# Kernel tuning notes

Hardware: AMD Instinct MI355X
Metric: run time of the kernel (lower is better)

Reference implementation:

```python
import jax, jax.numpy as jnp
import numpy as np

N = 50000   # nodes (single node type)
E = 200000  # edges per relation
R = 2       # relations (etypes)
D = 256     # in_dim == out_dim
H = 8       # heads
DK = D // H # 32
SQRT_DK = float(np.sqrt(DK))


def setup_inputs() -> dict:
    key = jax.random.key(0)
    ks = jax.random.split(key, 12)
    wsc = 1.0 / np.sqrt(D)   # linear-layer scale
    rsc = 1.0 / np.sqrt(DK)  # xavier-ish scale for relation tensors
    return {
        "x": jax.random.normal(ks[0], (N, D), jnp.float32),
        "src": jax.random.randint(ks[1], (R, E), 0, N, jnp.int32),
        "dst": jax.random.randint(ks[2], (R, E), 0, N, jnp.int32),
        "Wk": jax.random.normal(ks[3], (D, D), jnp.float32) * wsc,
        "bk": jnp.zeros((D,), jnp.float32),
        "Wq": jax.random.normal(ks[4], (D, D), jnp.float32) * wsc,
        "bq": jnp.zeros((D,), jnp.float32),
        "Wv": jax.random.normal(ks[5], (D, D), jnp.float32) * wsc,
        "bv": jnp.zeros((D,), jnp.float32),
        "Wa": jax.random.normal(ks[6], (D, D), jnp.float32) * wsc,
        "ba": jnp.zeros((D,), jnp.float32),
        "rel_pri": jnp.ones((R, H), jnp.float32),
        "rel_att": jax.random.normal(ks[7], (R, H, DK, DK), jnp.float32) * rsc,
        "rel_msg": jax.random.normal(ks[8], (R, H, DK, DK), jnp.float32) * rsc,
        "skip": jnp.ones((1,), jnp.float32),
    }


def reference(x, src, dst, Wk, bk, Wq, bq, Wv, bv, Wa, ba, rel_pri, rel_att, rel_msg, skip):
    # Per-type K/Q/V projections (single node type) -> [N,H,DK]
    k = (x @ Wk + bk).reshape(N, H, DK)
    q = (x @ Wq + bq).reshape(N, H, DK)
    v = (x @ Wv + bv).reshape(N, H, DK)

    # edge_attention: per-relation bmm transform of gathered src features
    key_t = jnp.einsum('rehd,rhdf->rehf', k[src], rel_att)   # [R,E,H,DK]
    val = jnp.einsum('rehd,rhdf->rehf', v[src], rel_msg)     # [R,E,H,DK]
    att = (q[dst] * key_t).sum(-1) * rel_pri[:, None, :] / SQRT_DK  # [R,E,H]

    # segment softmax over incoming edges per (relation, dst node)
    seg = (dst + N * jnp.arange(R, dtype=dst.dtype)[:, None]).reshape(-1)  # [R*E]
    att_f = att.reshape(R * E, H)
    m = jax.ops.segment_max(att_f, seg, num_segments=R * N)
    m = jnp.where(jnp.isfinite(m), m, 0.0)  # empty segments -> never gathered
    e = jnp.exp(att_f - m[seg])
    den = jax.ops.segment_sum(e, seg, num_segments=R * N)
    attn = e / den[seg]                                       # [R*E,H]

    # weighted-sum scatter aggregation, then cross_reducer='mean' over relations
    h = jax.ops.segment_sum(attn[:, :, None] * val.reshape(R * E, H, DK), seg,
                            num_segments=R * N)               # [R*N,H,DK]
    t = h.reshape(R, N, D).mean(axis=0)                        # [N,D]

    # skip-gated output projection (dropout inactive in eval, use_norm=False)
    alpha = jax.nn.sigmoid(skip[0])
    return (t @ Wa + ba) * alpha + x * (1.0 - alpha)
```

## Files before the change

kernel.cpp:

```cpp
#include <hip/hip_runtime.h>
#include <hip/hip_bf16.h>
#include <math.h>

#define NN 50000
#define EE 200000
#define DD 256
#define HH 8
#define DKK 32
#define NSEG (2 * NN)
#define SCAN_BLOCKS ((NSEG + 1023) / 1024)
#define MPAD 50048
#define LDQKV 1280
#define CAST_BLOCKS 12500
#define COUNT_BLOCKS ((2 * EE + 255) / 256)

constexpr float RSQRT_DK = 0.17677669529663687f;

__device__ __forceinline__ float bf_lo(unsigned u) { return __uint_as_float(u << 16); }
__device__ __forceinline__ float bf_hi(unsigned u) { return __uint_as_float(u & 0xffff0000u); }
__device__ __forceinline__ unsigned short f2bf(float f) {
    unsigned u = __float_as_uint(f);
    return (unsigned short)((u + 0x7fffu + ((u >> 16) & 1u)) >> 16);
}

typedef __attribute__((ext_vector_type(8))) short bf16x8;
typedef __attribute__((ext_vector_type(4))) float f32x4;
typedef __attribute__((ext_vector_type(4))) unsigned int u32x4;

#define GLDS16(g, l)                                                                   \
    __builtin_amdgcn_global_load_lds((const __attribute__((address_space(1))) unsigned int*)(g), \
                                     (__attribute__((address_space(3))) unsigned int*)(l), 16, 0, 0)

__global__ void prep_kernel(const float* __restrict__ x, unsigned short* __restrict__ xb,
                            const float* __restrict__ Wq, const float* __restrict__ Wk,
                            const float* __restrict__ Wv, const float* __restrict__ bq,
                            const float* __restrict__ bk, const float* __restrict__ bv,
                            const float* __restrict__ rel_att, const float* __restrict__ rel_msg,
                            const float* __restrict__ Wa, unsigned short* __restrict__ wa_t,
                            unsigned short* __restrict__ Wt, float* __restrict__ bb,
                            const int* __restrict__ dst, int* __restrict__ cnt) {
    if (blockIdx.x < CAST_BLOCKS) {
        const size_t i = ((size_t)blockIdx.x * 256 + threadIdx.x) * 4;
        float4 v = *(const float4*)&x[i];
        ushort4 o;
        o.x = f2bf(v.x); o.y = f2bf(v.y); o.z = f2bf(v.z); o.w = f2bf(v.w);
        *(ushort4*)&xb[i] = o;
        return;
    }
    if (blockIdx.x >= CAST_BLOCKS + 1536) {
        const int e = (blockIdx.x - CAST_BLOCKS - 1536) * 256 + threadIdx.x;
        if (e < 2 * EE) atomicAdd(&cnt[(e >= EE ? NN : 0) + dst[e]], 1);
        return;
    }
    const int n = blockIdx.x - CAST_BLOCKS, kk = threadIdx.x;
    if (n >= 1280) {
        const int nn = n - 1280;
        wa_t[(size_t)nn * 256 + kk] = f2bf(Wa[(size_t)kk * 256 + nn]);
        return;
    }
    if (n < 256) {
        Wt[(size_t)n * 256 + kk] = f2bf(Wq[(size_t)kk * 256 + n]);
        if (kk == 0) bb[n] = bq[n];
        return;
    }
    const int sec = (n - 256) >> 8;
    const int c = (n - 256) & 255;
    const int h = c >> 5, f = c & 31;
    const float* W    = (sec < 2) ? Wk : Wv;
    const float* bsrc = (sec < 2) ? bk : bv;
    const float* T = ((sec < 2) ? rel_att : rel_msg)
                   + (size_t)(sec & 1) * HH * DKK * DKK + (size_t)h * DKK * DKK + f;
    const float* wrow = &W[(size_t)kk * 256 + h * 32];
    float s = 0.f;
    #pragma unroll
    for (int d = 0; d < 32; ++d) s += wrow[d] * T[(size_t)d * 32];
    Wt[(size_t)n * 256 + kk] = f2bf(s);
    if (kk == 0) {
        float sb = 0.f;
        for (int d = 0; d < 32; ++d) sb += bsrc[h * 32 + d] * T[(size_t)d * 32];
        bb[n] = sb;
    }
}

__global__ __launch_bounds__(256) void mfma_gemm(
        const unsigned short* __restrict__ A, const unsigned short* __restrict__ Bt,
        const float* __restrict__ bias,
        unsigned short* __restrict__ Cbf, float* __restrict__ Cf,
        int M, int ldc, const float* __restrict__ xres, const float* __restrict__ skip) {
    __shared__ __align__(16) unsigned short As[3][8][64][8];
    __shared__ __align__(16) unsigned short Bs[3][8][64][8];
    const int t = threadIdx.x;
    const int w = t >> 6, l = t & 63;

    const int nwg = gridDim.x * gridDim.y;
    int lin = blockIdx.y * gridDim.x + blockIdx.x;
    {
        const int xcd = lin & 7, pos = lin >> 3;
        const int q = nwg >> 3, r = nwg & 7;
        lin = (xcd < r ? xcd * (q + 1) : r * (q + 1) + (xcd - r) * q) + pos;
    }
    const int n0 = (lin % gridDim.x) * 128;
    const int m0 = (lin / gridDim.x) * 128;
    const int wm = w & 1, wn = w >> 1;

    const int sr = l & 15, sq = l >> 4;
    const unsigned short* ga0 = A  + (size_t)(m0 + w * 16 + sr) * 256 + sq * 8;
    const unsigned short* ga1 = A  + (size_t)(m0 + (w + 4) * 16 + sr) * 256 + sq * 8;
    const unsigned short* gb0 = Bt + (size_t)(n0 + w * 16 + sr) * 256 + sq * 8;
    const unsigned short* gb1 = Bt + (size_t)(n0 + (w + 4) * 16 + sr) * 256 + sq * 8;

#define STAGE(buf, k0) do {                    \
        GLDS16(ga0 + (k0), &As[buf][w][0][0]); \
        GLDS16(ga1 + (k0), &As[buf][w + 4][0][0]); \
        GLDS16(gb0 + (k0), &Bs[buf][w][0][0]); \
        GLDS16(gb1 + (k0), &Bs[buf][w + 4][0][0]); } while (0)

    f32x4 acc[4][4];
    #pragma unroll
    for (int mi = 0; mi < 4; ++mi)
        #pragma unroll
        for (int ni = 0; ni < 4; ++ni) acc[mi][ni] = (f32x4){0.f, 0.f, 0.f, 0.f};

    STAGE(0, 0);
    STAGE(1, 32);
    #pragma unroll
    for (int it = 0; it < 8; ++it) {
        if (it < 7) { asm volatile("s_waitcnt vmcnt(4)" ::: "memory"); }
        else        { asm volatile("s_waitcnt vmcnt(0)" ::: "memory"); }
        __builtin_amdgcn_s_barrier();
        __builtin_amdgcn_sched_barrier(0);
        if (it < 6) {
            STAGE((it + 2) % 3, (it + 2) * 32);
        }
        const int b = it % 3;
        bf16x8 af[4], bfr[4];
        #pragma unroll
        for (int i = 0; i < 4; ++i) {
            af[i]  = *(const bf16x8*)&As[b][wm * 4 + i][l][0];
            bfr[i] = *(const bf16x8*)&Bs[b][wn * 4 + i][l][0];
        }
        #pragma unroll
        for (int mi = 0; mi < 4; ++mi)
            #pragma unroll
            for (int ni = 0; ni < 4; ++ni)
                acc[mi][ni] = __builtin_amdgcn_mfma_f32_16x16x32_bf16(af[mi], bfr[ni],
                                                                      acc[mi][ni], 0, 0, 0);
    }
    __syncthreads();

    unsigned short* ep = (w < 2) ? &As[0][0][0][0] : &Bs[0][0][0][0];
    ep += (w & 1) * 4096;
    const int q4 = l >> 4, c15 = l & 15;

    if (Cf == nullptr) {
        #pragma unroll
        for (int ni = 0; ni < 4; ++ni) {
            const float bcol = bias[n0 + wn * 64 + ni * 16 + c15];
            const int g = ni * 2 + (c15 >> 3);
            #pragma unroll
            for (int mi = 0; mi < 4; ++mi)
                #pragma unroll
                for (int p = 0; p < 4; ++p) {
                    const int row = mi * 16 + q4 * 4 + p;
                    ep[row * 64 + ((g ^ (row & 7)) << 3) + (c15 & 7)] =
                        f2bf(acc[mi][ni][p] + bcol);
                }
        }
        __syncthreads();
        const int rs = l >> 3, cc = l & 7;
        #pragma unroll
        for (int i = 0; i < 8; ++i) {
            const int rl = i * 8 + rs;
            const int row = m0 + wm * 64 + rl;
            if (row < M) {
                u32x4 v = *(const u32x4*)&ep[rl * 64 + ((cc ^ (rl & 7)) << 3)];
                __builtin_nontemporal_store(v,
                    (u32x4*)&Cbf[(size_t)row * (size_t)ldc + n0 + wn * 64 + cc * 8]);
            }
        }
    } else {
        const float alpha = 1.f / (1.f + __expf(-skip[0]));
        const float beta = 1.f - alpha;
        float* epf = (float*)ep;
        #pragma unroll
        for (int half = 0; half < 2; ++half) {
            __syncthreads();
            #pragma unroll
            for (int mi2 = 0; mi2 < 2; ++mi2) {
                const int mi = half * 2 + mi2;
                #pragma unroll
                for (int ni = 0; ni < 4; ++ni) {
                    const float bcol = bias[n0 + wn * 64 + ni * 16 + c15];
                    const int g = ni * 4 + (c15 >> 2);
                    #pragma unroll
                    for (int p = 0; p < 4; ++p) {
                        const int row = mi2 * 16 + q4 * 4 + p;
                        epf[row * 64 + ((g ^ (row & 7)) << 2) + (c15 & 3)] =
                            acc[mi][ni][p] + bcol;
                    }
                }
            }
            __syncthreads();
            const int cc = l & 15, rs = l >> 4;
            #pragma unroll
            for (int i = 0; i < 8; ++i) {
                const int rl = i * 4 + rs;
                const int row = m0 + wm * 64 + half * 32 + rl;
                if (row < M) {
                    const int col = n0 + wn * 64 + cc * 4;
                    float4 v = *(const float4*)&epf[rl * 64 + ((cc ^ (rl & 7)) << 2)];
                    float4 xr = *(const float4*)&xres[(size_t)row * 256 + col];
                    f32x4 o;
                    o[0] = v.x * alpha + xr.x * beta;
                    o[1] = v.y * alpha + xr.y * beta;
                    o[2] = v.z * alpha + xr.z * beta;
                    o[3] = v.w * alpha + xr.w * beta;
                    __builtin_nontemporal_store(o, (f32x4*)&Cf[(size_t)row * 256 + col]);
                }
            }
        }
    }
#undef STAGE
}

__global__ __launch_bounds__(1024) void scan_local_kernel(const int* __restrict__ cnt,
                                                          int* __restrict__ rowptr,
                                                          int* __restrict__ bsum) {
    __shared__ int sh[1024];
    const int t = threadIdx.x;
    const int idx = blockIdx.x * 1024 + t;
    const int c = (idx < NSEG) ? cnt[idx] : 0;
    sh[t] = c;
    __syncthreads();
    #pragma unroll
    for (int ofs = 1; ofs < 1024; ofs <<= 1) {
        int v = (t >= ofs) ? sh[t - ofs] : 0;
        __syncthreads();
        sh[t] += v;
        __syncthreads();
    }
    if (idx < NSEG) rowptr[idx] = sh[t] - c;
    if (t == 1023) bsum[blockIdx.x] = sh[1023];
}

__global__ __launch_bounds__(1024) void scan_add_kernel(int* __restrict__ rowptr,
                                                        const int* __restrict__ bsum,
                                                        int* __restrict__ cursor) {
    __shared__ int sb[128];
    const int t = threadIdx.x;
    if (t < 128) sb[t] = (t < SCAN_BLOCKS) ? bsum[t] : 0;
    __syncthreads();
    #pragma unroll
    for (int ofs = 1; ofs < 128; ofs <<= 1) {
        int u = 0;
        if (t < 128 && t >= ofs) u = sb[t - ofs];
        __syncthreads();
        if (t < 128) sb[t] += u;
        __syncthreads();
    }
    const int pre = sb[blockIdx.x] - bsum[blockIdx.x];
    const int idx = blockIdx.x * 1024 + t;
    if (idx < NSEG) {
        const int v = rowptr[idx] + pre;
        rowptr[idx] = v;
        cursor[idx] = v;
    }
    if (blockIdx.x == 0 && t == 127) rowptr[NSEG] = sb[127];
}

__global__ void scatter_kernel(const int* __restrict__ src, const int* __restrict__ dst,
                               int* __restrict__ cursor, int* __restrict__ csr_src) {
    int e = blockIdx.x * 256 + threadIdx.x;
    if (e >= 2 * EE) return;
    int seg = (e / EE) * NN + dst[e];
    int pos = atomicAdd(&cursor[seg], 1);
    csr_src[pos] = src[e];
}

__global__ __launch_bounds__(512) void node_agg_kernel(
        const unsigned short* __restrict__ qkv,
        const int* __restrict__ csr_src,
        const int* __restrict__ rowptr,
        const float* __restrict__ pri,
        unsigned short* __restrict__ tt_bf) {
    __shared__ float sh[4][256];
    const int w = threadIdx.x >> 6, lane = threadIdx.x & 63;
    const int nl = w >> 1, r = w & 1;
    const int n = blockIdx.x * 4 + nl;
    const int lh = lane & 31;
    const int eh = lane >> 5;
    const int h = lh >> 2;
    const size_t coff = (size_t)lh * 8;

    const uint4 qv = *(const uint4*)&qkv[(size_t)n * LDQKV + coff];
    const float q0 = bf_lo(qv.x), q1 = bf_hi(qv.x), q2 = bf_lo(qv.y), q3 = bf_hi(qv.y);
    const float q4_ = bf_lo(qv.z), q5 = bf_hi(qv.z), q6 = bf_lo(qv.w), q7 = bf_hi(qv.w);

    const float prm = pri[r * HH + h] * RSQRT_DK;
    const int seg = r * NN + n;
    const int j0 = rowptr[seg], j1 = rowptr[seg + 1];
    const size_t kbase = 256 + (size_t)r * 256 + coff;
    const size_t vbase = 768 + (size_t)r * 256 + coff;

    float a0 = 0.f, a1 = 0.f, a2 = 0.f, a3 = 0.f, a4 = 0.f, a5 = 0.f, a6 = 0.f, a7 = 0.f;
    float den = 0.f;

    int j = j0 + eh;
    uint4 kv, vv;
    bool valid = j < j1;
    if (valid) {
        const size_t rowb = (size_t)csr_src[j] * LDQKV;
        kv = *(const uint4*)&qkv[rowb + kbase];
        vv = *(const uint4*)&qkv[rowb + vbase];
    }
    while (valid) {
        const int jn = j + 2;
        const bool validn = jn < j1;
        uint4 kvn, vvn;
        if (validn) {
            const size_t rowb = (size_t)csr_src[jn] * LDQKV;
            kvn = *(const uint4*)&qkv[rowb + kbase];
            vvn = *(const uint4*)&qkv[rowb + vbase];
        }
        float p = q0 * bf_lo(kv.x) + q1 * bf_hi(kv.x) + q2 * bf_lo(kv.y) + q3 * bf_hi(kv.y)
                + q4_ * bf_lo(kv.z) + q5 * bf_hi(kv.z) + q6 * bf_lo(kv.w) + q7 * bf_hi(kv.w);
        p += __shfl_xor(p, 1);
        p += __shfl_xor(p, 2);
        const float a = __expf(p * prm);
        den += a;
        a0 += a * bf_lo(vv.x); a1 += a * bf_hi(vv.x);
        a2 += a * bf_lo(vv.y); a3 += a * bf_hi(vv.y);
        a4 += a * bf_lo(vv.z); a5 += a * bf_hi(vv.z);
        a6 += a * bf_lo(vv.w); a7 += a * bf_hi(vv.w);
        kv = kvn; vv = vvn; j = jn; valid = validn;
    }
    den += __shfl_xor(den, 32);
    a0 += __shfl_xor(a0, 32); a1 += __shfl_xor(a1, 32);
    a2 += __shfl_xor(a2, 32); a3 += __shfl_xor(a3, 32);
    a4 += __shfl_xor(a4, 32); a5 += __shfl_xor(a5, 32);
    a6 += __shfl_xor(a6, 32); a7 += __shfl_xor(a7, 32);
    const float wgt = (den > 0.f) ? 0.5f / den : 0.f;

    if (r == 0 && eh == 0) {
        sh[nl][0 * 32 + lh] = a0 * wgt; sh[nl][1 * 32 + lh] = a1 * wgt;
        sh[nl][2 * 32 + lh] = a2 * wgt; sh[nl][3 * 32 + lh] = a3 * wgt;
        sh[nl][4 * 32 + lh] = a4 * wgt; sh[nl][5 * 32 + lh] = a5 * wgt;
        sh[nl][6 * 32 + lh] = a6 * wgt; sh[nl][7 * 32 + lh] = a7 * wgt;
    }
    __syncthreads();
    if (r == 1 && eh == 0) {
        const float t0 = sh[nl][0 * 32 + lh] + a0 * wgt;
        const float t1 = sh[nl][1 * 32 + lh] + a1 * wgt;
        const float t2 = sh[nl][2 * 32 + lh] + a2 * wgt;
        const float t3 = sh[nl][3 * 32 + lh] + a3 * wgt;
        const float t4 = sh[nl][4 * 32 + lh] + a4 * wgt;
        const float t5 = sh[nl][5 * 32 + lh] + a5 * wgt;
        const float t6 = sh[nl][6 * 32 + lh] + a6 * wgt;
        const float t7 = sh[nl][7 * 32 + lh] + a7 * wgt;
        uint4 o;
        o.x = (unsigned)f2bf(t0) | ((unsigned)f2bf(t1) << 16);
        o.y = (unsigned)f2bf(t2) | ((unsigned)f2bf(t3) << 16);
        o.z = (unsigned)f2bf(t4) | ((unsigned)f2bf(t5) << 16);
        o.w = (unsigned)f2bf(t6) | ((unsigned)f2bf(t7) << 16);
        *(uint4*)&tt_bf[(size_t)n * 256 + coff] = o;
    }
}

extern "C" void kernel_launch(void* const* d_in, const int* in_sizes, int n_in,
                              void* d_out, int out_size, void* d_ws, size_t ws_size,
                              hipStream_t stream) {
    const float* x       = (const float*)d_in[0];
    const int*   src     = (const int*)d_in[1];
    const int*   dst     = (const int*)d_in[2];
    const float* Wk      = (const float*)d_in[3];
    const float* bk      = (const float*)d_in[4];
    const float* Wq      = (const float*)d_in[5];
    const float* bq      = (const float*)d_in[6];
    const float* Wv      = (const float*)d_in[7];
    const float* bv      = (const float*)d_in[8];
    const float* Wa      = (const float*)d_in[9];
    const float* ba      = (const float*)d_in[10];
    const float* rel_pri = (const float*)d_in[11];
    const float* rel_att = (const float*)d_in[12];
    const float* rel_msg = (const float*)d_in[13];
    const float* skip    = (const float*)d_in[14];
    float* out = (float*)d_out;
    char* ws = (char*)d_ws;

    size_t off = 0;
    unsigned short* x_bf   = (unsigned short*)(ws + off); off += (size_t)MPAD * DD * 2;
    unsigned short* qkv_bf = (unsigned short*)(ws + off); off += (size_t)NN * LDQKV * 2;
    unsigned short* tt_bf  = (unsigned short*)(ws + off); off += (size_t)MPAD * DD * 2;
    unsigned short* wqkv_t = (unsigned short*)(ws + off); off += (size_t)LDQKV * 256 * 2;
    unsigned short* wa_t   = (unsigned short*)(ws + off); off += (size_t)256 * 256 * 2;
    float*          bb     = (float*)(ws + off);          off += LDQKV * 4;
    int*            cnt    = (int*)(ws + off);            off += (size_t)NSEG * 4;
    int*            rowptr = (int*)(ws + off);            off += (size_t)(NSEG + 1) * 4;
    int*            cursor = (int*)(ws + off);            off += (size_t)NSEG * 4;
    int*            bsum   = (int*)(ws + off);            off += 128 * 4;
    int*            csr_src= (int*)(ws + off);            off += (size_t)2 * EE * 4;
    if (ws_size < off) return;

    hipMemsetAsync(cnt, 0, (size_t)NSEG * 4, stream);

    prep_kernel<<<CAST_BLOCKS + 1536 + COUNT_BLOCKS, 256, 0, stream>>>(
        x, x_bf, Wq, Wk, Wv, bq, bk, bv, rel_att, rel_msg, Wa, wa_t, wqkv_t, bb,
        dst, cnt);

    dim3 g_qkv(LDQKV / 128, MPAD / 128);
    mfma_gemm<<<g_qkv, 256, 0, stream>>>(x_bf, wqkv_t, bb, qkv_bf, nullptr,
                                         NN, LDQKV, nullptr, nullptr);

    scan_local_kernel<<<SCAN_BLOCKS, 1024, 0, stream>>>(cnt, rowptr, bsum);
    scan_add_kernel<<<SCAN_BLOCKS, 1024, 0, stream>>>(rowptr, bsum, cursor);
    scatter_kernel<<<COUNT_BLOCKS, 256, 0, stream>>>(src, dst, cursor, csr_src);

    node_agg_kernel<<<NN / 4, 512, 0, stream>>>(qkv_bf, csr_src, rowptr,
                                                rel_pri, tt_bf);

    dim3 g_out(DD / 128, MPAD / 128);
    mfma_gemm<<<g_out, 256, 0, stream>>>(tt_bf, wa_t, ba, nullptr, out,
                                         NN, DD, x, skip);
}
```

Before: 370.8 us.

## Fold relation matrices into Q and output weights instead of K and V projections

The per-relation attention transform is now folded into the query projection (rel_att applied to Wq per relation), and the message transform is folded into the output projection (rel_msg times Wa stacked along K for both relations). As a result the QKV GEMM emits 1024 columns instead of 1280, and node aggregation writes separate per-relation results, so the cross-wave shared-memory reduction and the syncthreads are gone. The output GEMM is templated to a K of 512 to absorb the relation sum. The trade-off is a larger intermediate tensor (twice the tt_bf bytes written and then read) and double the K work in the final GEMM.

```diff
diff --git a/kernel.cpp b/kernel.cpp
--- a/kernel.cpp
+++ b/kernel.cpp
@@ -10,8 +10,10 @@
 #define NSEG (2 * NN)
 #define SCAN_BLOCKS ((NSEG + 1023) / 1024)
 #define MPAD 50048
-#define LDQKV 1280
+#define LDQKV 1024
 #define CAST_BLOCKS 12500
+#define FOLD_BLOCKS 1024
+#define WA2_BLOCKS 256
 #define COUNT_BLOCKS ((2 * EE + 255) / 256)
 
 constexpr float RSQRT_DK = 0.17677669529663687f;
@@ -36,57 +38,68 @@
                             const float* __restrict__ Wv, const float* __restrict__ bq,
                             const float* __restrict__ bk, const float* __restrict__ bv,
                             const float* __restrict__ rel_att, const float* __restrict__ rel_msg,
-                            const float* __restrict__ Wa, unsigned short* __restrict__ wa_t,
+                            const float* __restrict__ Wa, unsigned short* __restrict__ wa2_t,
                             unsigned short* __restrict__ Wt, float* __restrict__ bb,
                             const int* __restrict__ dst, int* __restrict__ cnt) {
+    const int kk = threadIdx.x;
     if (blockIdx.x < CAST_BLOCKS) {
-        const size_t i = ((size_t)blockIdx.x * 256 + threadIdx.x) * 4;
+        const size_t i = ((size_t)blockIdx.x * 256 + kk) * 4;
         float4 v = *(const float4*)&x[i];
         ushort4 o;
         o.x = f2bf(v.x); o.y = f2bf(v.y); o.z = f2bf(v.z); o.w = f2bf(v.w);
         *(ushort4*)&xb[i] = o;
         return;
     }
-    if (blockIdx.x >= CAST_BLOCKS + 1536) {
-        const int e = (blockIdx.x - CAST_BLOCKS - 1536) * 256 + threadIdx.x;
-        if (e < 2 * EE) atomicAdd(&cnt[(e >= EE ? NN : 0) + dst[e]], 1);
+    if (blockIdx.x < CAST_BLOCKS + FOLD_BLOCKS) {
+        const int n = blockIdx.x - CAST_BLOCKS;
+        if (n < 512) {
+            const int r = n >> 8, c = n & 255;
+            const int h = c >> 5, d = c & 31;
+            const float* T = rel_att + (size_t)((r * HH + h) * DKK + d) * DKK;
+            const float* wrow = &Wq[(size_t)kk * 256 + h * 32];
+            float s = 0.f;
+            #pragma unroll
+            for (int f = 0; f < 32; ++f) s += wrow[f] * T[f];
+            Wt[(size_t)n * 256 + kk] = f2bf(s);
+            if (kk == 0) {
+                float sb = 0.f;
+                for (int f = 0; f < 32; ++f) sb += bq[h * 32 + f] * T[f];
+                bb[n] = sb;
+            }
+        } else {
+            const int sec = (n - 512) >> 8;
+            const int c = (n - 512) & 255;
+            const float* W    = sec ? Wv : Wk;
+            const float* bsrc = sec ? bv : bk;
+            Wt[(size_t)n * 256 + kk] = f2bf(W[(size_t)kk * 256 + c]);
+            if (kk == 0) bb[n] = bsrc[c];
+        }
         return;
     }
-    const int n = blockIdx.x - CAST_BLOCKS, kk = threadIdx.x;
-    if (n >= 1280) {
-        const int nn = n - 1280;
-        wa_t[(size_t)nn * 256 + kk] = f2bf(Wa[(size_t)kk * 256 + nn]);
+    if (blockIdx.x < CAST_BLOCKS + FOLD_BLOCKS + WA2_BLOCKS) {
+        const int n = blockIdx.x - CAST_BLOCKS - FOLD_BLOCKS;
+        const int h = kk >> 5, d = kk & 31;
+        #pragma unroll
+        for (int r = 0; r < 2; ++r) {
+            const float* T = rel_msg + (size_t)((r * HH + h) * DKK + d) * DKK;
+            float s = 0.f;
+            #pragma unroll
+            for (int f = 0; f < 32; ++f) s += T[f] * Wa[(size_t)(h * 32 + f) * 256 + n];
+            wa2_t[(size_t)n * 512 + r * 256 + kk] = f2bf(s);
+        }
         return;
     }
-    if (n < 256) {
-        Wt[(size_t)n * 256 + kk] = f2bf(Wq[(size_t)kk * 256 + n]);
-        if (kk == 0) bb[n] = bq[n];
-        return;
-    }
-    const int sec = (n - 256) >> 8;
-    const int c = (n - 256) & 255;
-    const int h = c >> 5, f = c & 31;
-    const float* W    = (sec < 2) ? Wk : Wv;
-    const float* bsrc = (sec < 2) ? bk : bv;
-    const float* T = ((sec < 2) ? rel_att : rel_msg)
-                   + (size_t)(sec & 1) * HH * DKK * DKK + (size_t)h * DKK * DKK + f;
-    const float* wrow = &W[(size_t)kk * 256 + h * 32];
-    float s = 0.f;
-    #pragma unroll
-    for (int d = 0; d < 32; ++d) s += wrow[d] * T[(size_t)d * 32];
-    Wt[(size_t)n * 256 + kk] = f2bf(s);
-    if (kk == 0) {
-        float sb = 0.f;
-        for (int d = 0; d < 32; ++d) sb += bsrc[h * 32 + d] * T[(size_t)d * 32];
-        bb[n] = sb;
-    }
-}
-
+    const int e = (blockIdx.x - CAST_BLOCKS - FOLD_BLOCKS - WA2_BLOCKS) * 256 + kk;
+    if (e < 2 * EE) atomicAdd(&cnt[(e >= EE ? NN : 0) + dst[e]], 1);
+}
+
+template <int KI>
 __global__ __launch_bounds__(256) void mfma_gemm(
         const unsigned short* __restrict__ A, const unsigned short* __restrict__ Bt,
         const float* __restrict__ bias,
         unsigned short* __restrict__ Cbf, float* __restrict__ Cf,
         int M, int ldc, const float* __restrict__ xres, const float* __restrict__ skip) {
+    constexpr int K = KI * 32;
     __shared__ __align__(16) unsigned short As[3][8][64][8];
     __shared__ __align__(16) unsigned short Bs[3][8][64][8];
     const int t = threadIdx.x;
@@ -104,10 +117,10 @@
     const int wm = w & 1, wn = w >> 1;
 
     const int sr = l & 15, sq = l >> 4;
-    const unsigned short* ga0 = A  + (size_t)(m0 + w * 16 + sr) * 256 + sq * 8;
-    const unsigned short* ga1 = A  + (size_t)(m0 + (w + 4) * 16 + sr) * 256 + sq * 8;
-    const unsigned short* gb0 = Bt + (size_t)(n0 + w * 16 + sr) * 256 + sq * 8;
-    const unsigned short* gb1 = Bt + (size_t)(n0 + (w + 4) * 16 + sr) * 256 + sq * 8;
+    const unsigned short* ga0 = A  + (size_t)(m0 + w * 16 + sr) * K + sq * 8;
+    const unsigned short* ga1 = A  + (size_t)(m0 + (w + 4) * 16 + sr) * K + sq * 8;
+    const unsigned short* gb0 = Bt + (size_t)(n0 + w * 16 + sr) * K + sq * 8;
+    const unsigned short* gb1 = Bt + (size_t)(n0 + (w + 4) * 16 + sr) * K + sq * 8;
 
 #define STAGE(buf, k0) do {                    \
         GLDS16(ga0 + (k0), &As[buf][w][0][0]); \
@@ -124,12 +137,12 @@
     STAGE(0, 0);
     STAGE(1, 32);
     #pragma unroll
-    for (int it = 0; it < 8; ++it) {
-        if (it < 7) { asm volatile("s_waitcnt vmcnt(4)" ::: "memory"); }
-        else        { asm volatile("s_waitcnt vmcnt(0)" ::: "memory"); }
+    for (int it = 0; it < KI; ++it) {
+        if (it < KI - 1) { asm volatile("s_waitcnt vmcnt(4)" ::: "memory"); }
+        else             { asm volatile("s_waitcnt vmcnt(0)" ::: "memory"); }
         __builtin_amdgcn_s_barrier();
         __builtin_amdgcn_sched_barrier(0);
-        if (it < 6) {
+        if (it < KI - 2) {
             STAGE((it + 2) % 3, (it + 2) * 32);
         }
         const int b = it % 3;
@@ -283,7 +296,6 @@
         const int* __restrict__ rowptr,
         const float* __restrict__ pri,
         unsigned short* __restrict__ tt_bf) {
-    __shared__ float sh[4][256];
     const int w = threadIdx.x >> 6, lane = threadIdx.x & 63;
     const int nl = w >> 1, r = w & 1;
     const int n = blockIdx.x * 4 + nl;
@@ -292,15 +304,15 @@
     const int h = lh >> 2;
     const size_t coff = (size_t)lh * 8;
 
-    const uint4 qv = *(const uint4*)&qkv[(size_t)n * LDQKV + coff];
+    const uint4 qv = *(const uint4*)&qkv[(size_t)n * LDQKV + r * 256 + coff];
     const float q0 = bf_lo(qv.x), q1 = bf_hi(qv.x), q2 = bf_lo(qv.y), q3 = bf_hi(qv.y);
     const float q4_ = bf_lo(qv.z), q5 = bf_hi(qv.z), q6 = bf_lo(qv.w), q7 = bf_hi(qv.w);
 
     const float prm = pri[r * HH + h] * RSQRT_DK;
     const int seg = r * NN + n;
     const int j0 = rowptr[seg], j1 = rowptr[seg + 1];
-    const size_t kbase = 256 + (size_t)r * 256 + coff;
-    const size_t vbase = 768 + (size_t)r * 256 + coff;
+    const size_t kbase = 512 + coff;
+    const size_t vbase = 768 + coff;
 
     float a0 = 0.f, a1 = 0.f, a2 = 0.f, a3 = 0.f, a4 = 0.f, a5 = 0.f, a6 = 0.f, a7 = 0.f;
     float den = 0.f;
@@ -341,28 +353,13 @@
     a6 += __shfl_xor(a6, 32); a7 += __shfl_xor(a7, 32);
     const float wgt = (den > 0.f) ? 0.5f / den : 0.f;
 
-    if (r == 0 && eh == 0) {
-        sh[nl][0 * 32 + lh] = a0 * wgt; sh[nl][1 * 32 + lh] = a1 * wgt;
-        sh[nl][2 * 32 + lh] = a2 * wgt; sh[nl][3 * 32 + lh] = a3 * wgt;
-        sh[nl][4 * 32 + lh] = a4 * wgt; sh[nl][5 * 32 + lh] = a5 * wgt;
-        sh[nl][6 * 32 + lh] = a6 * wgt; sh[nl][7 * 32 + lh] = a7 * wgt;
-    }
-    __syncthreads();
-    if (r == 1 && eh == 0) {
-        const float t0 = sh[nl][0 * 32 + lh] + a0 * wgt;
-        const float t1 = sh[nl][1 * 32 + lh] + a1 * wgt;
-        const float t2 = sh[nl][2 * 32 + lh] + a2 * wgt;
-        const float t3 = sh[nl][3 * 32 + lh] + a3 * wgt;
-        const float t4 = sh[nl][4 * 32 + lh] + a4 * wgt;
-        const float t5 = sh[nl][5 * 32 + lh] + a5 * wgt;
-        const float t6 = sh[nl][6 * 32 + lh] + a6 * wgt;
-        const float t7 = sh[nl][7 * 32 + lh] + a7 * wgt;
+    if (eh == 0) {
         uint4 o;
-        o.x = (unsigned)f2bf(t0) | ((unsigned)f2bf(t1) << 16);
-        o.y = (unsigned)f2bf(t2) | ((unsigned)f2bf(t3) << 16);
-        o.z = (unsigned)f2bf(t4) | ((unsigned)f2bf(t5) << 16);
-        o.w = (unsigned)f2bf(t6) | ((unsigned)f2bf(t7) << 16);
-        *(uint4*)&tt_bf[(size_t)n * 256 + coff] = o;
+        o.x = (unsigned)f2bf(a0 * wgt) | ((unsigned)f2bf(a1 * wgt) << 16);
+        o.y = (unsigned)f2bf(a2 * wgt) | ((unsigned)f2bf(a3 * wgt) << 16);
+        o.z = (unsigned)f2bf(a4 * wgt) | ((unsigned)f2bf(a5 * wgt) << 16);
+        o.w = (unsigned)f2bf(a6 * wgt) | ((unsigned)f2bf(a7 * wgt) << 16);
+        *(uint4*)&tt_bf[(size_t)n * 512 + r * 256 + coff] = o;
     }
 }
 
@@ -390,9 +387,9 @@
     size_t off = 0;
     unsigned short* x_bf   = (unsigned short*)(ws + off); off += (size_t)MPAD * DD * 2;
     unsigned short* qkv_bf = (unsigned short*)(ws + off); off += (size_t)NN * LDQKV * 2;
-    unsigned short* tt_bf  = (unsigned short*)(ws + off); off += (size_t)MPAD * DD * 2;
+    unsigned short* tt_bf  = (unsigned short*)(ws + off); off += (size_t)MPAD * 512 * 2;
     unsigned short* wqkv_t = (unsigned short*)(ws + off); off += (size_t)LDQKV * 256 * 2;
-    unsigned short* wa_t   = (unsigned short*)(ws + off); off += (size_t)256 * 256 * 2;
+    unsigned short* wa2_t  = (unsigned short*)(ws + off); off += (size_t)256 * 512 * 2;
     float*          bb     = (float*)(ws + off);          off += LDQKV * 4;
     int*            cnt    = (int*)(ws + off);            off += (size_t)NSEG * 4;
     int*            rowptr = (int*)(ws + off);            off += (size_t)(NSEG + 1) * 4;
@@ -403,13 +400,13 @@
 
     hipMemsetAsync(cnt, 0, (size_t)NSEG * 4, stream);
 
-    prep_kernel<<<CAST_BLOCKS + 1536 + COUNT_BLOCKS, 256, 0, stream>>>(
-        x, x_bf, Wq, Wk, Wv, bq, bk, bv, rel_att, rel_msg, Wa, wa_t, wqkv_t, bb,
+    prep_kernel<<<CAST_BLOCKS + FOLD_BLOCKS + WA2_BLOCKS + COUNT_BLOCKS, 256, 0, stream>>>(
+        x, x_bf, Wq, Wk, Wv, bq, bk, bv, rel_att, rel_msg, Wa, wa2_t, wqkv_t, bb,
         dst, cnt);
 
     dim3 g_qkv(LDQKV / 128, MPAD / 128);
-    mfma_gemm<<<g_qkv, 256, 0, stream>>>(x_bf, wqkv_t, bb, qkv_bf, nullptr,
-                                         NN, LDQKV, nullptr, nullptr);
+    mfma_gemm<8><<<g_qkv, 256, 0, stream>>>(x_bf, wqkv_t, bb, qkv_bf, nullptr,
+                                            NN, LDQKV, nullptr, nullptr);
 
     scan_local_kernel<<<SCAN_BLOCKS, 1024, 0, stream>>>(cnt, rowptr, bsum);
     scan_add_kernel<<<SCAN_BLOCKS, 1024, 0, stream>>>(rowptr, bsum, cursor);
@@ -419,6 +416,6 @@
                                                 rel_pri, tt_bf);
 
     dim3 g_out(DD / 128, MPAD / 128);
-    mfma_gemm<<<g_out, 256, 0, stream>>>(tt_bf, wa_t, ba, nullptr, out,
-                                         NN, DD, x, skip);
-}
+    mfma_gemm<16><<<g_out, 256, 0, stream>>>(tt_bf, wa2_t, ba, nullptr, out,
+                                             NN, DD, x, skip);
+}
```

Result: no change. 369.7 us (-0.3%).
